# Performance work log

Hardware: AMD Instinct MI355X
Metric: run time of the kernel (lower is better)

## Reference

```python
import jax, jax.numpy as jnp
import numpy as np

# Material constants (from init_kwargs: E=1e4, nu=0.3)
E_MOD = 1.0e4
NU = 0.3
MU = E_MOD / (2.0 * (1.0 + NU))                      # shear modulus
LMBDA = E_MOD * NU / ((1.0 + NU) * (1.0 - 2.0 * NU))  # first Lame parameter
EPS = 1e-10

B, N_NODES, N_ELEM, N_QUAD, NPE = 4, 100000, 500000, 4, 4  # tet4 mesh


def setup_inputs() -> dict:
    key = jax.random.key(0)
    k1, k2, k3, k4 = jax.random.split(key, 4)
    # small displacements so J = det(I + grad_u) stays positive
    u = jax.random.normal(k1, (B, N_NODES, 3), dtype=jnp.float32) * 0.01
    elements = jax.random.randint(k2, (N_ELEM, NPE), 0, N_NODES)
    # precomputed shape-function derivatives dN/dx per element/quad point
    dN_dx = jax.random.normal(k3, (N_ELEM, N_QUAD, NPE, 3), dtype=jnp.float32) * 0.1
    # positive Jacobian determinants of the reference->physical map
    detJ = jax.random.uniform(k4, (N_ELEM, N_QUAD), dtype=jnp.float32, minval=0.5, maxval=1.5) * 1e-3
    # tet4 4-point quadrature weights: 0.25 / 6
    quad_weights = jnp.full((N_QUAD,), 0.25 / 6.0, dtype=jnp.float32)
    return {"u": u, "elements": elements, "dN_dx": dN_dx, "detJ": detJ,
            "quad_weights": quad_weights}


def reference(u, elements, dN_dx, detJ, quad_weights):
    # gather nodal displacements per element: [B, E, n, 3]
    elem_u = u[:, elements]
    # grad_u[b,e,q,i,j] = sum_n elem_u[b,e,n,i] * dN_dx[e,q,n,j]  -> [B,E,Q,3,3]
    grad_u = jnp.einsum('beni,eqnj->beqij', elem_u, dN_dx)
    F = grad_u + jnp.eye(3, dtype=u.dtype)
    J = jnp.linalg.det(F)                      # [B,E,Q]
    I_C = jnp.sum(F * F, axis=(-2, -1))        # tr(F^T F)
    logJ = jnp.log(jnp.maximum(J, EPS))
    W = 0.5 * MU * (I_C - 3.0 - 2.0 * logJ) + 0.25 * LMBDA * (J * J - 1.0 - 2.0 * logJ)
    # quadrature-weighted assembly over elements and quad points -> [B]
    return jnp.einsum('beq,eq,q->b', W, detJ, quad_weights)
```

## Files before the change

kernel.cpp:

```cpp
#include <hip/hip_runtime.h>

#define MU_C   3846.1538461538462f
#define LM_C   5769.2307692307695f
#define LOGC   (MU_C + 0.5f * LM_C)
#define EPS_C  1e-10f

#define KPT 4
#define TILE (64 * KPT)

__global__ __launch_bounds__(256) void nh_transpose_u_pad(
    const float* __restrict__ u, float4* __restrict__ ut, int n_nodes)
{
    const int i = blockIdx.x * 256 + threadIdx.x;
    if (i >= n_nodes) return;
    float4* q = ut + (size_t)i * 4;
    #pragma unroll
    for (int b = 0; b < 4; ++b) {
        const float* p = u + ((size_t)b * n_nodes + i) * 3;
        q[b] = make_float4(p[0], p[1], p[2], 0.f);
    }
}

__device__ __forceinline__ float nh_energy(
    const float4* dn,
    const float4* uu,
    const float*  wqv)
{
    const float* d  = reinterpret_cast<const float*>(dn);
    const float* us = reinterpret_cast<const float*>(uu);
    float a = 0.f;
    #pragma unroll
    for (int q = 0; q < 4; ++q) {
        float F[3][3];
        #pragma unroll
        for (int i = 0; i < 3; ++i) {
            #pragma unroll
            for (int j = 0; j < 3; ++j) {
                float g = 0.f;
                #pragma unroll
                for (int n = 0; n < 4; ++n)
                    g = fmaf(us[n * 4 + i], d[(q*4 + n)*3 + j], g);
                F[i][j] = g + ((i == j) ? 1.f : 0.f);
            }
        }
        const float J =
              F[0][0] * (F[1][1]*F[2][2] - F[1][2]*F[2][1])
            - F[0][1] * (F[1][0]*F[2][2] - F[1][2]*F[2][0])
            + F[0][2] * (F[1][0]*F[2][1] - F[1][1]*F[2][0]);
        float IC = 0.f;
        #pragma unroll
        for (int i = 0; i < 3; ++i)
            #pragma unroll
            for (int j = 0; j < 3; ++j)
                IC = fmaf(F[i][j], F[i][j], IC);
        const float lj = __logf(fmaxf(J, EPS_C));
        const float W = 0.5f * MU_C * (IC - 3.f)
                      + 0.25f * LM_C * fmaf(J, J, -1.f)
                      - LOGC * lj;
        a = fmaf(W, wqv[q], a);
    }
    return a;
}

__global__ __launch_bounds__(256) void nh_partial_v6(
    const float4* __restrict__ ut,
    const int*    __restrict__ elements,
    const float*  __restrict__ dN_dx,
    const float*  __restrict__ detJ,
    const float*  __restrict__ qw,
    float* __restrict__ partial,
    int n_elem)
{
    const int t = threadIdx.x;
    const int b = t & 3;
    const int p = t >> 2;
    const int base = blockIdx.x * TILE + p;

    const int4*   elp = reinterpret_cast<const int4*>(elements);
    const float4* djp = reinterpret_cast<const float4*>(detJ);
    const float4* dnp = reinterpret_cast<const float4*>(dN_dx);
    const float4  w4  = *reinterpret_cast<const float4*>(qw);

    int4   nd[2];
    float4 dj[2];
    float4 dn[2][12];
    float4 uu[2][4];
    float  wqv[2][4];

    #define NH_LOAD(S, M)                                                     \
    {                                                                         \
        const int e  = base + (M) * 64;                                       \
        const int ec = min(e, n_elem - 1);                                    \
        const bool valid = (e < n_elem);                                      \
        nd[S] = elp[ec];                                                      \
        dj[S] = djp[ec];                                                      \
        const float4* dptr = dnp + (size_t)ec * 12;                           \
        _Pragma("unroll")                                                     \
        for (int k = 0; k < 12; ++k) dn[S][k] = dptr[k];                      \
        const int* ndp = reinterpret_cast<const int*>(&nd[S]);                \
        _Pragma("unroll")                                                     \
        for (int n = 0; n < 4; ++n)                                           \
            uu[S][n] = ut[(size_t)ndp[n] * 4 + b];                            \
        const float vs = valid ? 1.f : 0.f;                                   \
        wqv[S][0] = dj[S].x * w4.x * vs;                                      \
        wqv[S][1] = dj[S].y * w4.y * vs;                                      \
        wqv[S][2] = dj[S].z * w4.z * vs;                                      \
        wqv[S][3] = dj[S].w * w4.w * vs;                                      \
    }

    float acc = 0.f;

    NH_LOAD(0, 0)
    NH_LOAD(1, 1)

    #pragma unroll
    for (int m = 0; m < KPT; ++m) {
        const int s = m & 1;
        acc += nh_energy(dn[s], uu[s], wqv[s]);
        if (m + 2 < KPT) {
            if (s == 0) { NH_LOAD(0, m + 2) } else { NH_LOAD(1, m + 2) }
        }
    }
    #undef NH_LOAD

    #pragma unroll
    for (int off = 32; off >= 4; off >>= 1)
        acc += __shfl_down(acc, off);

    __shared__ float s_red[4][4];
    const int lane = t & 63;
    const int wid  = t >> 6;
    if (lane < 4) s_red[wid][lane] = acc;
    __syncthreads();
    if (t < 4)
        partial[(size_t)blockIdx.x * 4 + t] =
            (s_red[0][t] + s_red[1][t]) + (s_red[2][t] + s_red[3][t]);
}

__global__ __launch_bounds__(256) void nh_final(
    const float* __restrict__ partial,
    float* __restrict__ out,
    int nparts)
{
    float accb[4] = {0.f, 0.f, 0.f, 0.f};
    for (int i = threadIdx.x; i < nparts; i += 256) {
        const float4 p = reinterpret_cast<const float4*>(partial)[i];
        accb[0] += p.x; accb[1] += p.y; accb[2] += p.z; accb[3] += p.w;
    }

    #pragma unroll
    for (int b = 0; b < 4; ++b) {
        float v = accb[b];
        #pragma unroll
        for (int off = 32; off > 0; off >>= 1)
            v += __shfl_down(v, off);
        accb[b] = v;
    }

    __shared__ float lds[4][4];
    const int lane = threadIdx.x & 63;
    const int wid  = threadIdx.x >> 6;
    if (lane == 0) {
        #pragma unroll
        for (int b = 0; b < 4; ++b) lds[wid][b] = accb[b];
    }
    __syncthreads();
    if (threadIdx.x == 0) {
        #pragma unroll
        for (int b = 0; b < 4; ++b)
            out[b] = (lds[0][b] + lds[1][b]) + (lds[2][b] + lds[3][b]);
    }
}

extern "C" void kernel_launch(void* const* d_in, const int* in_sizes, int n_in,
                              void* d_out, int out_size, void* d_ws, size_t ws_size,
                              hipStream_t stream) {
    const float* u        = (const float*)d_in[0];
    const int*   elements = (const int*)d_in[1];
    const float* dN_dx    = (const float*)d_in[2];
    const float* detJ     = (const float*)d_in[3];
    const float* qw       = (const float*)d_in[4];
    float* out = (float*)d_out;

    const int B       = out_size;
    const int n_nodes = in_sizes[0] / (3 * B);
    const int n_elem  = in_sizes[1] / 4;

    const int threads = 256;
    const int nblocks = (n_elem + TILE - 1) / TILE;

    const size_t ut_bytes      = (size_t)n_nodes * 4 * sizeof(float4);
    float4* ut     = (float4*)d_ws;
    float* partial = (float*)((char*)d_ws + ut_bytes);

    const int tb = (n_nodes + threads - 1) / threads;
    nh_transpose_u_pad<<<tb, threads, 0, stream>>>(u, ut, n_nodes);

    nh_partial_v6<<<nblocks, threads, 0, stream>>>(ut, elements, dN_dx, detJ, qw,
                                                   partial, n_elem);
    nh_final<<<1, threads, 0, stream>>>(partial, out, nblocks);
}
```

Before: 57.96 us.

## Switch partial kernel to grid-stride loop with occupancy hint, drop manual double-buffering

Replaces the fixed 4-elements-per-thread tile and its explicit two-stage register prefetch with a grid-stride loop over 64-element tiles, using a capped grid of 2048 blocks. Adds a launch-bounds minimum-blocks hint to push register use down so more waves are resident. The aim is to hide gather latency through occupancy instead of software pipelining and to shrink the number of partial sums. The cost is losing explicit load/compute overlap within each thread, plus possible spills if the register cap is too tight.

```diff
diff --git a/kernel.cpp b/kernel.cpp
--- a/kernel.cpp
+++ b/kernel.cpp
@@ -5,8 +5,7 @@
 #define LOGC   (MU_C + 0.5f * LM_C)
 #define EPS_C  1e-10f
 
-#define KPT 4
-#define TILE (64 * KPT)
+#define PBLOCKS 2048
 
 __global__ __launch_bounds__(256) void nh_transpose_u_pad(
     const float* __restrict__ u, float4* __restrict__ ut, int n_nodes)
@@ -62,66 +61,48 @@
     return a;
 }
 
-__global__ __launch_bounds__(256) void nh_partial_v6(
+__global__ __launch_bounds__(256, 7) void nh_partial_v7(
     const float4* __restrict__ ut,
     const int*    __restrict__ elements,
     const float*  __restrict__ dN_dx,
     const float*  __restrict__ detJ,
     const float*  __restrict__ qw,
     float* __restrict__ partial,
-    int n_elem)
+    int n_elem, int ntiles)
 {
     const int t = threadIdx.x;
     const int b = t & 3;
     const int p = t >> 2;
-    const int base = blockIdx.x * TILE + p;
 
     const int4*   elp = reinterpret_cast<const int4*>(elements);
     const float4* djp = reinterpret_cast<const float4*>(detJ);
     const float4* dnp = reinterpret_cast<const float4*>(dN_dx);
     const float4  w4  = *reinterpret_cast<const float4*>(qw);
 
-    int4   nd[2];
-    float4 dj[2];
-    float4 dn[2][12];
-    float4 uu[2][4];
-    float  wqv[2][4];
-
-    #define NH_LOAD(S, M)                                                     \
-    {                                                                         \
-        const int e  = base + (M) * 64;                                       \
-        const int ec = min(e, n_elem - 1);                                    \
-        const bool valid = (e < n_elem);                                      \
-        nd[S] = elp[ec];                                                      \
-        dj[S] = djp[ec];                                                      \
-        const float4* dptr = dnp + (size_t)ec * 12;                           \
-        _Pragma("unroll")                                                     \
-        for (int k = 0; k < 12; ++k) dn[S][k] = dptr[k];                      \
-        const int* ndp = reinterpret_cast<const int*>(&nd[S]);                \
-        _Pragma("unroll")                                                     \
-        for (int n = 0; n < 4; ++n)                                           \
-            uu[S][n] = ut[(size_t)ndp[n] * 4 + b];                            \
-        const float vs = valid ? 1.f : 0.f;                                   \
-        wqv[S][0] = dj[S].x * w4.x * vs;                                      \
-        wqv[S][1] = dj[S].y * w4.y * vs;                                      \
-        wqv[S][2] = dj[S].z * w4.z * vs;                                      \
-        wqv[S][3] = dj[S].w * w4.w * vs;                                      \
-    }
-
     float acc = 0.f;
 
-    NH_LOAD(0, 0)
-    NH_LOAD(1, 1)
+    for (int tile = blockIdx.x; tile < ntiles; tile += gridDim.x) {
+        const int e = tile * 64 + p;
+        if (e >= n_elem) continue;
 
-    #pragma unroll
-    for (int m = 0; m < KPT; ++m) {
-        const int s = m & 1;
-        acc += nh_energy(dn[s], uu[s], wqv[s]);
-        if (m + 2 < KPT) {
-            if (s == 0) { NH_LOAD(0, m + 2) } else { NH_LOAD(1, m + 2) }
-        }
+        const int4   nd = elp[e];
+        const float4 dj = djp[e];
+
+        float4 dv[12];
+        const float4* dptr = dnp + (size_t)e * 12;
+        #pragma unroll
+        for (int k = 0; k < 12; ++k) dv[k] = dptr[k];
+
+        float4 uu[4];
+        uu[0] = ut[nd.x * 4 + b];
+        uu[1] = ut[nd.y * 4 + b];
+        uu[2] = ut[nd.z * 4 + b];
+        uu[3] = ut[nd.w * 4 + b];
+
+        const float wqv[4] = {dj.x * w4.x, dj.y * w4.y, dj.z * w4.z, dj.w * w4.w};
+
+        acc += nh_energy(dv, uu, wqv);
     }
-    #undef NH_LOAD
 
     #pragma unroll
     for (int off = 32; off >= 4; off >>= 1)
@@ -187,16 +168,17 @@
     const int n_elem  = in_sizes[1] / 4;
 
     const int threads = 256;
-    const int nblocks = (n_elem + TILE - 1) / TILE;
+    const int ntiles  = (n_elem + 63) / 64;
+    const int nblocks = (ntiles < PBLOCKS) ? ntiles : PBLOCKS;
 
-    const size_t ut_bytes      = (size_t)n_nodes * 4 * sizeof(float4);
+    const size_t ut_bytes = (size_t)n_nodes * 4 * sizeof(float4);
     float4* ut     = (float4*)d_ws;
     float* partial = (float*)((char*)d_ws + ut_bytes);
 
     const int tb = (n_nodes + threads - 1) / threads;
     nh_transpose_u_pad<<<tb, threads, 0, stream>>>(u, ut, n_nodes);
 
-    nh_partial_v6<<<nblocks, threads, 0, stream>>>(ut, elements, dN_dx, detJ, qw,
-                                                   partial, n_elem);
+    nh_partial_v7<<<nblocks, threads, 0, stream>>>(ut, elements, dN_dx, detJ, qw,
+                                                   partial, n_elem, ntiles);
     nh_final<<<1, threads, 0, stream>>>(partial, out, nblocks);
 }
```

Measured after the change: 86.44 us. 49.1% more time.
